# Optimization experiments

Measured on AMD Instinct MI355X. Metric: run time of the kernel, lower is better.

The kernel has to match this reference:

```python
import jax, jax.numpy as jnp
import numpy as np

B, T, C = 2, 2048, 2048
N_HEAD, N_KV_HEAD = 16, 4
HEAD_DIM = C // N_HEAD  # 128
HALF = HEAD_DIM // 2    # 64


def _rms_norm(x):
    # F.rms_norm with no weight: x / sqrt(mean(x^2) + eps), eps = dtype eps
    eps = jnp.finfo(x.dtype).eps
    return x * jax.lax.rsqrt(jnp.mean(x * x, axis=-1, keepdims=True) + eps)


def _rope_apply(x, cos, sin):
    # x: [B, H, T, Hs]; cos/sin: [1, 1, T, Hs/2]
    x1, x2 = x[..., :HALF], x[..., HALF:]
    return jnp.concatenate([x1 * cos - x2 * sin, x1 * sin + x2 * cos], axis=-1)


def setup_inputs() -> dict:
    key = jax.random.key(0)
    ks = jax.random.split(key, 8)
    x = jax.random.normal(ks[0], (B, T, C), dtype=jnp.float32)
    # real RoPE tables (base 10000), shape [1,1,T,HALF]
    inv_freq = 1.0 / (10000.0 ** (np.arange(0, HALF, dtype=np.float32) / HALF))
    t = np.arange(T, dtype=np.float32)
    ang = np.einsum('t,f->tf', t, inv_freq)
    cos = jnp.asarray(np.cos(ang))[None, None]
    sin = jnp.asarray(np.sin(ang))[None, None]
    s = 0.02
    Wq = jax.random.normal(ks[1], (C, N_HEAD * HEAD_DIM), dtype=jnp.float32) * s
    Wk = jax.random.normal(ks[2], (C, N_KV_HEAD * HEAD_DIM), dtype=jnp.float32) * s
    Wv = jax.random.normal(ks[3], (C, N_KV_HEAD * HEAD_DIM), dtype=jnp.float32) * s
    Wo = jax.random.normal(ks[4], (C, C), dtype=jnp.float32) * s
    bo = jnp.zeros((C,), dtype=jnp.float32)
    return {"x": x, "cos": cos, "sin": sin, "Wq": Wq, "Wk": Wk, "Wv": Wv, "Wo": Wo, "bo": bo}


def reference(x, cos, sin, Wq, Wk, Wv, Wo, bo):
    Bq, Tq, Cq = x.shape
    G = N_HEAD // N_KV_HEAD
    # QKV projections (GQA, no bias)
    q = (x @ Wq).reshape(Bq, Tq, N_HEAD, HEAD_DIM)
    k = (x @ Wk).reshape(Bq, Tq, N_KV_HEAD, HEAD_DIM)
    v = (x @ Wv).reshape(Bq, Tq, N_KV_HEAD, HEAD_DIM)
    # QK RMSNorm (over head_dim), then to [B, H, T, Hs]
    q = jnp.transpose(_rms_norm(q), (0, 2, 1, 3))
    k = jnp.transpose(_rms_norm(k), (0, 2, 1, 3))
    v = jnp.transpose(v, (0, 2, 1, 3))
    # RoPE
    q = _rope_apply(q, cos[:, :, :Tq, :], sin[:, :, :Tq, :])
    k = _rope_apply(k, cos[:, :, :Tq, :], sin[:, :, :Tq, :])
    # GQA: repeat kv heads across groups
    k = jnp.repeat(k, G, axis=1)  # [B, H, T, Hs]
    v = jnp.repeat(v, G, axis=1)
    # Causal SDPA
    scale = 1.0 / jnp.sqrt(jnp.asarray(HEAD_DIM, dtype=x.dtype))
    scores = jnp.einsum('bhqd,bhkd->bhqk', q, k) * scale
    causal = jnp.tril(jnp.ones((Tq, Tq), dtype=bool))
    scores = jnp.where(causal, scores, jnp.asarray(-jnp.inf, dtype=scores.dtype))
    attn = jax.nn.softmax(scores, axis=-1)
    y = jnp.einsum('bhqk,bhkd->bhqd', attn, v)
    y = jnp.transpose(y, (0, 2, 1, 3)).reshape(Bq, Tq, Cq)
    return y @ Wo + bo
```

## Files before the change

### kernel.cpp

```cpp
#include <hip/hip_runtime.h>
#include <hip/hip_bf16.h>
#include <math.h>

#define BB 2
#define TT 2048
#define CC 2048
#define NH 16
#define NKV 4
#define HD 128
#define HALF 64
#define MTOT (BB*TT)
#define NQKV (CC + 2*NKV*HD)

typedef unsigned short u16;
typedef __attribute__((ext_vector_type(8))) short bf16x8;
typedef __attribute__((ext_vector_type(4))) float f32x4;

__device__ __forceinline__ u16 f2bf(float f) {
  unsigned u = __float_as_uint(f);
  unsigned r = (u + 0x7FFFu + ((u >> 16) & 1u)) >> 16;
  return (u16)r;
}
__device__ __forceinline__ float bf2f(u16 v) {
  return __uint_as_float(((unsigned)v) << 16);
}

__device__ __forceinline__ void gl_lds16(const void* g, void* l) {
  __builtin_amdgcn_global_load_lds(
      (const __attribute__((address_space(1))) unsigned int*)g,
      (__attribute__((address_space(3))) unsigned int*)l, 16, 0, 0);
}

__global__ __launch_bounds__(256) void prep(
    const float* __restrict__ x, const float* __restrict__ Wq,
    const float* __restrict__ Wk, const float* __restrict__ Wv,
    const float* __restrict__ Wo, u16* __restrict__ xb,
    u16* __restrict__ Wt, u16* __restrict__ Wot) {
  const int z = blockIdx.z;
  const int tx = threadIdx.x, ty = threadIdx.y;
  if (z == 4) {
    const int tid = ty * 32 + tx;
    const int i = (blockIdx.y * 64 + blockIdx.x) * 256 + tid;
    const float4* s4 = (const float4*)x;
    float4 a = s4[(size_t)i * 2], b = s4[(size_t)i * 2 + 1];
    bf16x8 o;
    o[0] = (short)f2bf(a.x); o[1] = (short)f2bf(a.y);
    o[2] = (short)f2bf(a.z); o[3] = (short)f2bf(a.w);
    o[4] = (short)f2bf(b.x); o[5] = (short)f2bf(b.y);
    o[6] = (short)f2bf(b.z); o[7] = (short)f2bf(b.w);
    ((bf16x8*)xb)[i] = o;
    return;
  }
  const float* W; u16* dst; int N; int row_off;
  if (z == 0)      { W = Wq; dst = Wt;  N = 2048; row_off = 0; }
  else if (z == 1) { W = Wk; dst = Wt;  N = 512;  row_off = 2048; }
  else if (z == 2) { W = Wv; dst = Wt;  N = 512;  row_off = 2560; }
  else             { W = Wo; dst = Wot; N = 2048; row_off = 0; }
  const int n0 = blockIdx.x * 32, k0 = blockIdx.y * 32;
  if (n0 >= N) return;
  __shared__ float tile[32][33];
#pragma unroll
  for (int i = 0; i < 4; ++i)
    tile[ty + 8 * i][tx] = W[(size_t)(k0 + ty + 8 * i) * N + n0 + tx];
  __syncthreads();
#pragma unroll
  for (int i = 0; i < 4; ++i)
    dst[(size_t)(row_off + n0 + ty + 8 * i) * CC + k0 + tx] =
        f2bf(tile[tx][ty + 8 * i]);
}

__global__ __launch_bounds__(512, 2) void gemm_8ph(
    const u16* __restrict__ A, const u16* __restrict__ Bt,
    const float* __restrict__ bias, float* __restrict__ C,
    int M, int N, int K, int out_bf16) {
  __shared__ u16 As[32768];
  __shared__ u16 Bs[32768];
  const int tid = threadIdx.x;
  const int w = tid >> 6, lane = tid & 63;
  const int quad = lane >> 4, lo = lane & 15;
  const int wm = w >> 2, wn = w & 3;
  const int bm = blockIdx.y * 256, bn = blockIdx.x * 256;
  const int NT = K >> 6;

  const u16* agp[2][2]; const u16* bgp[2][2];
#pragma unroll
  for (int h = 0; h < 2; ++h)
#pragma unroll
    for (int j = 0; j < 2; ++j) {
      const unsigned X = (unsigned)h * 16384u +
                         (unsigned)((w * 2 + j) * 64 + lane) * 16u;
      const int row = (int)(X >> 7);
      const int ce = (int)(((X & 127u) ^ (((X >> 7) & 7u) << 4)) >> 1);
      agp[h][j] = A  + (size_t)(bm + row) * K + ce;
      bgp[h][j] = Bt + (size_t)(bn + row) * K + ce;
    }
  char* const lAs = (char*)As;
  char* const lBs = (char*)Bs;
  const int woff = w * 2048;

#define STGA(hh, bufp, kt) do { \
    gl_lds16(agp[hh][0] + (size_t)(kt) * 64, lAs + (bufp) * 32768 + (hh) * 16384 + woff); \
    gl_lds16(agp[hh][1] + (size_t)(kt) * 64, lAs + (bufp) * 32768 + (hh) * 16384 + woff + 1024); \
  } while (0)
#define STGB(hh, bufp, kt) do { \
    gl_lds16(bgp[hh][0] + (size_t)(kt) * 64, lBs + (bufp) * 32768 + (hh) * 16384 + woff); \
    gl_lds16(bgp[hh][1] + (size_t)(kt) * 64, lBs + (bufp) * 32768 + (hh) * 16384 + woff + 1024); \
  } while (0)

  const int sw  = (lo & 7) << 4;
  const int co0 = (quad * 16) ^ sw;
  const int co1 = (64 + quad * 16) ^ sw;
  const int aRB = (wm * 128 + lo) * 128;
  const int bRB = (wn * 64 + lo) * 128;

  f32x4 acc[8][4];
#pragma unroll
  for (int ri = 0; ri < 8; ++ri)
#pragma unroll
    for (int ci = 0; ci < 4; ++ci)
#pragma unroll
      for (int r = 0; r < 4; ++r) acc[ri][ci][r] = 0.f;

  STGA(0, 0, 0); STGA(1, 0, 0); STGB(0, 0, 0); STGB(1, 0, 0);
  STGB(0, 1, 1); STGB(1, 1, 1); STGA(0, 1, 1);
  asm volatile("s_waitcnt vmcnt(6)" ::: "memory");
  __builtin_amdgcn_s_barrier();

  for (int t = 0; t < NT; ++t) {
    const int pa = t & 1;
    const char* Ab = lAs + pa * 32768 + aRB;
    const char* Bb = lBs + pa * 32768 + bRB;
    bf16x8 a[4][2], b0[2][2], b1[2][2];

#pragma unroll
    for (int i = 0; i < 4; ++i) {
      a[i][0] = *(const bf16x8*)(Ab + i * 2048 + co0);
      a[i][1] = *(const bf16x8*)(Ab + i * 2048 + co1);
    }
#pragma unroll
    for (int j = 0; j < 2; ++j) {
      b0[j][0] = *(const bf16x8*)(Bb + j * 2048 + co0);
      b0[j][1] = *(const bf16x8*)(Bb + j * 2048 + co1);
    }
    if (t + 1 < NT) STGA(1, (t + 1) & 1, t + 1);
    __builtin_amdgcn_s_barrier();
    asm volatile("s_waitcnt lgkmcnt(0)");
    __builtin_amdgcn_s_setprio(1);
#pragma unroll
    for (int i = 0; i < 4; ++i)
#pragma unroll
      for (int j = 0; j < 2; ++j) {
        acc[i][j] = __builtin_amdgcn_mfma_f32_16x16x32_bf16(a[i][0], b0[j][0], acc[i][j], 0, 0, 0);
        acc[i][j] = __builtin_amdgcn_mfma_f32_16x16x32_bf16(a[i][1], b0[j][1], acc[i][j], 0, 0, 0);
      }
    __builtin_amdgcn_s_setprio(0);
    __builtin_amdgcn_s_barrier();

#pragma unroll
    for (int j = 0; j < 2; ++j) {
      b1[j][0] = *(const bf16x8*)(Bb + 4096 + j * 2048 + co0);
      b1[j][1] = *(const bf16x8*)(Bb + 4096 + j * 2048 + co1);
    }
    __builtin_amdgcn_s_barrier();
    asm volatile("s_waitcnt lgkmcnt(0)");
    __builtin_amdgcn_s_setprio(1);
#pragma unroll
    for (int i = 0; i < 4; ++i)
#pragma unroll
      for (int j = 0; j < 2; ++j) {
        acc[i][2 + j] = __builtin_amdgcn_mfma_f32_16x16x32_bf16(a[i][0], b1[j][0], acc[i][2 + j], 0, 0, 0);
        acc[i][2 + j] = __builtin_amdgcn_mfma_f32_16x16x32_bf16(a[i][1], b1[j][1], acc[i][2 + j], 0, 0, 0);
      }
    __builtin_amdgcn_s_setprio(0);
    __builtin_amdgcn_s_barrier();

#pragma unroll
    for (int i = 0; i < 4; ++i) {
      a[i][0] = *(const bf16x8*)(Ab + 8192 + i * 2048 + co0);
      a[i][1] = *(const bf16x8*)(Ab + 8192 + i * 2048 + co1);
    }
    if (t + 2 < NT) STGB(0, pa, t + 2);
    __builtin_amdgcn_s_barrier();
    asm volatile("s_waitcnt lgkmcnt(0)");
    __builtin_amdgcn_s_setprio(1);
#pragma unroll
    for (int i = 0; i < 4; ++i)
#pragma unroll
      for (int j = 0; j < 2; ++j) {
        acc[4 + i][2 + j] = __builtin_amdgcn_mfma_f32_16x16x32_bf16(a[i][0], b1[j][0], acc[4 + i][2 + j], 0, 0, 0);
        acc[4 + i][2 + j] = __builtin_amdgcn_mfma_f32_16x16x32_bf16(a[i][1], b1[j][1], acc[4 + i][2 + j], 0, 0, 0);
      }
    __builtin_amdgcn_s_setprio(0);
    __builtin_amdgcn_s_barrier();

    if (t + 2 < NT) { STGB(1, pa, t + 2); STGA(0, pa, t + 2); }
    if (t + 2 < NT)      asm volatile("s_waitcnt vmcnt(6)" ::: "memory");
    else if (t + 1 < NT) asm volatile("s_waitcnt vmcnt(0)" ::: "memory");
    __builtin_amdgcn_s_barrier();
    asm volatile("s_waitcnt lgkmcnt(0)");
    __builtin_amdgcn_s_setprio(1);
#pragma unroll
    for (int i = 0; i < 4; ++i)
#pragma unroll
      for (int j = 0; j < 2; ++j) {
        acc[4 + i][j] = __builtin_amdgcn_mfma_f32_16x16x32_bf16(a[i][0], b0[j][0], acc[4 + i][j], 0, 0, 0);
        acc[4 + i][j] = __builtin_amdgcn_mfma_f32_16x16x32_bf16(a[i][1], b0[j][1], acc[4 + i][j], 0, 0, 0);
      }
    __builtin_amdgcn_s_setprio(0);
    __builtin_amdgcn_s_barrier();
  }
#undef STGA
#undef STGB

  const int rbase = bm + wm * 128;
  const int cbase = bn + wn * 64;
#pragma unroll
  for (int ri = 0; ri < 8; ++ri)
#pragma unroll
    for (int ci = 0; ci < 4; ++ci) {
      const int col = cbase + ci * 16 + lo;
      const float bv = bias ? bias[col] : 0.f;
#pragma unroll
      for (int r = 0; r < 4; ++r) {
        const int row = rbase + ri * 16 + quad * 4 + r;
        const float v = acc[ri][ci][r] + bv;
        if (out_bf16) ((u16*)C)[(size_t)row * N + col] = f2bf(v);
        else          C[(size_t)row * N + col] = v;
      }
    }
}

__global__ __launch_bounds__(512, 2) void gemm_n128(
    const u16* __restrict__ A, const u16* __restrict__ Bt,
    const float* __restrict__ bias, float* __restrict__ C,
    int M, int N, int K, int out_bf16) {
  __shared__ u16 As[32768];
  __shared__ u16 Bs[16384];
  const int tid = threadIdx.x;
  const int w = tid >> 6, lane = tid & 63;
  const int quad = lane >> 4, lo = lane & 15;
  const int wm = w >> 1, wn = w & 1;
  const int bm = blockIdx.y * 256, bn = blockIdx.x * 128;
  const int NT = K >> 6;

  const u16* agp[2][2];
#pragma unroll
  for (int h = 0; h < 2; ++h)
#pragma unroll
    for (int j = 0; j < 2; ++j) {
      const unsigned X = (unsigned)h * 16384u +
                         (unsigned)((w * 2 + j) * 64 + lane) * 16u;
      const int row = (int)(X >> 7);
      const int ce = (int)(((X & 127u) ^ (((X >> 7) & 7u) << 4)) >> 1);
      agp[h][j] = A + (size_t)(bm + row) * K + ce;
    }
  const u16* bgp[2];
#pragma unroll
  for (int j = 0; j < 2; ++j) {
    const unsigned X = (unsigned)((w * 2 + j) * 64 + lane) * 16u;
    const int row = (int)(X >> 7);
    const int ce = (int)(((X & 127u) ^ (((X >> 7) & 7u) << 4)) >> 1);
    bgp[j] = Bt + (size_t)(bn + row) * K + ce;
  }
  char* const lAs = (char*)As;
  char* const lBs = (char*)Bs;
  const int woff = w * 2048;

#define STGA_(hh, bufp, kt) do { \
    gl_lds16(agp[hh][0] + (size_t)(kt) * 64, lAs + (bufp) * 32768 + (hh) * 16384 + woff); \
    gl_lds16(agp[hh][1] + (size_t)(kt) * 64, lAs + (bufp) * 32768 + (hh) * 16384 + woff + 1024); \
  } while (0)
#define STGB_(bufp, kt) do { \
    gl_lds16(bgp[0] + (size_t)(kt) * 64, lBs + (bufp) * 16384 + woff); \
    gl_lds16(bgp[1] + (size_t)(kt) * 64, lBs + (bufp) * 16384 + woff + 1024); \
  } while (0)

  const int sw  = (lo & 7) << 4;
  const int co0 = (quad * 16) ^ sw;
  const int co1 = (64 + quad * 16) ^ sw;
  const int aRB = (wm * 64 + lo) * 128;
  const int bRB = (wn * 64 + lo) * 128;

  f32x4 acc[4][4];
#pragma unroll
  for (int i = 0; i < 4; ++i)
#pragma unroll
    for (int ci = 0; ci < 4; ++ci)
#pragma unroll
      for (int r = 0; r < 4; ++r) acc[i][ci][r] = 0.f;

  STGA_(0, 0, 0); STGA_(1, 0, 0); STGB_(0, 0);
  STGB_(1, 1); STGA_(0, 1, 1);
  asm volatile("s_waitcnt vmcnt(4)" ::: "memory");
  __builtin_amdgcn_s_barrier();

  for (int t = 0; t < NT; ++t) {
    const int pa = t & 1;
    const char* Ab = lAs + pa * 32768 + aRB;
    const char* Bb = lBs + pa * 16384 + bRB;
    bf16x8 a[4][2], b[4][2];
#pragma unroll
    for (int i = 0; i < 4; ++i) {
      a[i][0] = *(const bf16x8*)(Ab + i * 2048 + co0);
      a[i][1] = *(const bf16x8*)(Ab + i * 2048 + co1);
    }
#pragma unroll
    for (int ci = 0; ci < 4; ++ci) {
      b[ci][0] = *(const bf16x8*)(Bb + ci * 2048 + co0);
      b[ci][1] = *(const bf16x8*)(Bb + ci * 2048 + co1);
    }
    if (t + 1 < NT) STGA_(1, (t + 1) & 1, t + 1);
    asm volatile("s_waitcnt lgkmcnt(0)");
    __builtin_amdgcn_s_barrier();
    __builtin_amdgcn_s_setprio(1);
#pragma unroll
    for (int i = 0; i < 4; ++i)
#pragma unroll
      for (int ci = 0; ci < 2; ++ci) {
        acc[i][ci] = __builtin_amdgcn_mfma_f32_16x16x32_bf16(a[i][0], b[ci][0], acc[i][ci], 0, 0, 0);
        acc[i][ci] = __builtin_amdgcn_mfma_f32_16x16x32_bf16(a[i][1], b[ci][1], acc[i][ci], 0, 0, 0);
      }
    __builtin_amdgcn_s_setprio(0);
    if (t + 2 < NT) { STGB_(pa, t + 2); STGA_(0, pa, t + 2); }
    if (t + 2 < NT)      asm volatile("s_waitcnt vmcnt(4)" ::: "memory");
    else if (t + 1 < NT) asm volatile("s_waitcnt vmcnt(0)" ::: "memory");
    __builtin_amdgcn_s_setprio(1);
#pragma unroll
    for (int i = 0; i < 4; ++i)
#pragma unroll
      for (int ci = 2; ci < 4; ++ci) {
        acc[i][ci] = __builtin_amdgcn_mfma_f32_16x16x32_bf16(a[i][0], b[ci][0], acc[i][ci], 0, 0, 0);
        acc[i][ci] = __builtin_amdgcn_mfma_f32_16x16x32_bf16(a[i][1], b[ci][1], acc[i][ci], 0, 0, 0);
      }
    __builtin_amdgcn_s_setprio(0);
    __builtin_amdgcn_s_barrier();
  }
#undef STGA_
#undef STGB_

  const int rbase = bm + wm * 64;
  const int cbase = bn + wn * 64;
#pragma unroll
  for (int i = 0; i < 4; ++i)
#pragma unroll
    for (int ci = 0; ci < 4; ++ci) {
      const int col = cbase + ci * 16 + lo;
      const float bv = bias ? bias[col] : 0.f;
#pragma unroll
      for (int r = 0; r < 4; ++r) {
        const int row = rbase + i * 16 + quad * 4 + r;
        const float v = acc[i][ci][r] + bv;
        if (out_bf16) ((u16*)C)[(size_t)row * N + col] = f2bf(v);
        else          C[(size_t)row * N + col] = v;
      }
    }
}

__global__ __launch_bounds__(256) void qkv_post(
    const u16* __restrict__ qkv_lin, const float* __restrict__ cosp,
    const float* __restrict__ sinp, u16* __restrict__ q, u16* __restrict__ k) {
  const int bt = blockIdx.x;
  const int hh = blockIdx.y * 4 + (threadIdx.x >> 6);
  const int lane = threadIdx.x & 63;
  const int t = bt & (TT - 1), b = bt >> 11;
  const int col = (hh < NH) ? hh * HD : CC + (hh - NH) * HD;
  const u16* src = qkv_lin + (size_t)bt * NQKV + col;
  float v1 = bf2f(src[lane]), v2 = bf2f(src[lane + 64]);
  float ss = v1 * v1 + v2 * v2;
#pragma unroll
  for (int mm = 1; mm < 64; mm <<= 1) ss += __shfl_xor(ss, mm, 64);
  float rms = rsqrtf(ss * (1.f / 128.f) + 1.1920929e-7f);
  float c = cosp[t * HALF + lane], s = sinp[t * HALF + lane];
  float o1 = v1 * rms * c - v2 * rms * s;
  float o2 = v1 * rms * s + v2 * rms * c;
  if (hh < NH) {
    u16* dst = q + (((size_t)(b * NH + hh)) * TT + t) * HD;
    dst[lane] = f2bf(o1); dst[lane + 64] = f2bf(o2);
  } else {
    u16* dst = k + (((size_t)(b * NKV + (hh - NH))) * TT + t) * HD;
    dst[lane] = f2bf(o1); dst[lane + 64] = f2bf(o2);
  }
}

__global__ __launch_bounds__(256) void v_transpose(
    const u16* __restrict__ qkv_lin, u16* __restrict__ vt) {
  __shared__ u16 tile[32][33];
  const int t0 = blockIdx.x * 32, d0 = blockIdx.y * 32;
  const int p = blockIdx.z;
  const int b = p >> 2, kv = p & 3;
  const int tx = threadIdx.x, ty = threadIdx.y;
#pragma unroll
  for (int i = 0; i < 4; ++i)
    tile[ty + 8 * i][tx] =
        qkv_lin[(size_t)(b * TT + t0 + ty + 8 * i) * NQKV + CC + NKV * HD + kv * HD + d0 + tx];
  __syncthreads();
  const int tperm = ((tx >> 2) & 3) * 8 + (tx & 3) + 4 * ((tx >> 4) & 1);
#pragma unroll
  for (int i = 0; i < 4; ++i)
    vt[((size_t)p * HD + d0 + ty + 8 * i) * TT + t0 + tperm] = tile[tx][ty + 8 * i];
}

__device__ __forceinline__ void softmax_pack(
    const f32x4* sacc, float& l_lane, bf16x8* ap, int rowq, int t0,
    bool diag, int quad) {
  const float cc = 0.12751744050808612f;
  float e[4][4];
  if (diag) {
#pragma unroll
    for (int ct = 0; ct < 4; ++ct)
#pragma unroll
      for (int r = 0; r < 4; ++r) {
        float v = __builtin_amdgcn_exp2f(sacc[ct][r] * cc);
        if (t0 + ct * 16 + quad * 4 + r > rowq) v = 0.f;
        l_lane += v; e[ct][r] = v;
      }
  } else {
#pragma unroll
    for (int ct = 0; ct < 4; ++ct)
#pragma unroll
      for (int r = 0; r < 4; ++r) {
        float v = __builtin_amdgcn_exp2f(sacc[ct][r] * cc);
        l_lane += v; e[ct][r] = v;
      }
  }
#pragma unroll
  for (int k2 = 0; k2 < 2; ++k2) {
    bf16x8 ch;
#pragma unroll
    for (int j = 0; j < 8; ++j)
      ch[j] = (short)f2bf(e[k2 * 2 + (j >> 2)][j & 3]);
    ap[k2] = ch;
  }
}

__global__ __launch_bounds__(256, 2) void attn_mfma(
    const u16* __restrict__ Qb, const u16* __restrict__ Kb,
    const u16* __restrict__ Vt, u16* __restrict__ Y) {
  __shared__ u16 Ks[2][8192];
  __shared__ u16 Vs[2][8192];

  const int qt = blockIdx.x;
  const int bh = blockIdx.y;
  const int b = bh >> 4, h = bh & 15, kvh = h >> 2;
  const int tid = threadIdx.x;
  const int wave = tid >> 6, lane = tid & 63;
  const int quad = lane >> 4, lo = lane & 15;

  const int rowsA = qt * 64, rowsB = (31 - qt) * 64;
  const u16* Qg = Qb + (size_t)(b * NH + h) * TT * HD;
  const u16* Kg = Kb + (size_t)(b * NKV + kvh) * TT * HD;
  const u16* Vg = Vt + (size_t)(b * NKV + kvh) * HD * TT;

  bf16x8 aq[2][4];
#pragma unroll
  for (int kc = 0; kc < 4; ++kc) {
    aq[0][kc] = *(const bf16x8*)(Qg + (size_t)(rowsA + wave * 16 + lo) * HD + kc * 32 + quad * 8);
    aq[1][kc] = *(const bf16x8*)(Qg + (size_t)(rowsB + wave * 16 + lo) * HD + kc * 32 + quad * 8);
  }

  const u16* kgp[4]; const u16* vgp[4];
  u16* klp[2][4]; u16* vlp[2][4];
#pragma unroll
  for (int c = 0; c < 4; ++c) {
    const int s = wave * 4 + c;
    const int ct = s >> 2, kq = s & 3;
    kgp[c] = Kg + (size_t)(ct * 16 + lo) * HD + kq * 32 + quad * 8;
    const int dt = s >> 1, k2 = s & 1;
    vgp[c] = Vg + (size_t)(dt * 16 + lo) * TT + k2 * 32 + quad * 8;
    klp[0][c] = &Ks[0][s * 512]; klp[1][c] = &Ks[1][s * 512];
    vlp[0][c] = &Vs[0][s * 512]; vlp[1][c] = &Vs[1][s * 512];
  }

  f32x4 oacc[2][8];
#pragma unroll
  for (int rb = 0; rb < 2; ++rb)
#pragma unroll
    for (int dt = 0; dt < 8; ++dt)
#pragma unroll
      for (int r = 0; r < 4; ++r) oacc[rb][dt][r] = 0.f;
  float l_lane[2] = {0.f, 0.f};

  const int ntiles = 32 - qt;
  const int rowqA = rowsA + wave * 16 + lo;
  const int rowqB = rowsB + wave * 16 + lo;

#pragma unroll
  for (int c = 0; c < 4; ++c) {
    gl_lds16(kgp[c], klp[0][c]); kgp[c] += 64 * HD;
    gl_lds16(vgp[c], vlp[0][c]); vgp[c] += 64;
  }

  for (int nt = 0; nt < ntiles; ++nt) {
    const int par = nt & 1;
    __syncthreads();
    if (nt + 1 < ntiles) {
#pragma unroll
      for (int c = 0; c < 4; ++c) {
        gl_lds16(kgp[c], klp[par ^ 1][c]); kgp[c] += 64 * HD;
        gl_lds16(vgp[c], vlp[par ^ 1][c]); vgp[c] += 64;
      }
    }
    const u16* ksb = Ks[par];
    const u16* vsb = Vs[par];
    const int t0 = nt * 64;
    const bool act0 = (nt <= qt);

    f32x4 sacc[2][4];
#pragma unroll
    for (int rb = 0; rb < 2; ++rb)
#pragma unroll
      for (int ct = 0; ct < 4; ++ct)
#pragma unroll
        for (int r = 0; r < 4; ++r) sacc[rb][ct][r] = 0.f;
#pragma unroll
    for (int ct = 0; ct < 4; ++ct)
#pragma unroll
      for (int kc = 0; kc < 4; ++kc) {
        bf16x8 bk = *(const bf16x8*)&ksb[(ct * 4 + kc) * 512 + lane * 8];
        sacc[1][ct] = __builtin_amdgcn_mfma_f32_16x16x32_bf16(bk, aq[1][kc], sacc[1][ct], 0, 0, 0);
        if (act0)
          sacc[0][ct] = __builtin_amdgcn_mfma_f32_16x16x32_bf16(bk, aq[0][kc], sacc[0][ct], 0, 0, 0);
      }

    bf16x8 ap[2][2];
    softmax_pack(sacc[1], l_lane[1], ap[1], rowqB, t0,
                 t0 + 63 > rowsB + wave * 16, quad);
    if (act0)
      softmax_pack(sacc[0], l_lane[0], ap[0], rowqA, t0,
                   t0 + 63 > rowsA + wave * 16, quad);

#pragma unroll
    for (int dt = 0; dt < 8; ++dt)
#pragma unroll
      for (int k2 = 0; k2 < 2; ++k2) {
        bf16x8 bv = *(const bf16x8*)&vsb[(dt * 2 + k2) * 512 + lane * 8];
        oacc[1][dt] = __builtin_amdgcn_mfma_f32_16x16x32_bf16(ap[1][k2], bv, oacc[1][dt], 0, 0, 0);
        if (act0)
          oacc[0][dt] = __builtin_amdgcn_mfma_f32_16x16x32_bf16(ap[0][k2], bv, oacc[0][dt], 0, 0, 0);
      }
  }

  float linv[2][4];
#pragma unroll
  for (int rb = 0; rb < 2; ++rb) {
    float l = l_lane[rb];
    l += __shfl_xor(l, 16, 64);
    l += __shfl_xor(l, 32, 64);
    l = 1.f / l;
#pragma unroll
    for (int r = 0; r < 4; ++r)
      linv[rb][r] = __shfl(l, quad * 4 + r, 64);
  }
#pragma unroll
  for (int rb = 0; rb < 2; ++rb) {
    const int rows = (rb == 0) ? rowsA : rowsB;
    const size_t row0 = (size_t)b * TT + rows + wave * 16 + quad * 4;
#pragma unroll
    for (int dt = 0; dt < 8; ++dt)
#pragma unroll
      for (int r = 0; r < 4; ++r)
        Y[(row0 + r) * CC + h * HD + dt * 16 + lo] = f2bf(oacc[rb][dt][r] * linv[rb][r]);
  }
}

extern "C" void kernel_launch(void* const* d_in, const int* in_sizes, int n_in,
                              void* d_out, int out_size, void* d_ws, size_t ws_size,
                              hipStream_t stream) {
  (void)in_sizes; (void)n_in; (void)out_size; (void)ws_size;
  const float* x    = (const float*)d_in[0];
  const float* cosp = (const float*)d_in[1];
  const float* sinp = (const float*)d_in[2];
  const float* Wq   = (const float*)d_in[3];
  const float* Wk   = (const float*)d_in[4];
  const float* Wv   = (const float*)d_in[5];
  const float* Wo   = (const float*)d_in[6];
  const float* bo   = (const float*)d_in[7];
  float* out = (float*)d_out;
  char* ws = (char*)d_ws;

  const size_t MB = 1024 * 1024;
  u16* xb      = (u16*)(ws);
  u16* Wt      = (u16*)(ws + 16 * MB);
  u16* qkv_lin = (u16*)(ws + 28 * MB);
  u16* Wot     = (u16*)(ws + 52 * MB);
  u16* qb_buf  = (u16*)(ws);
  u16* kb      = (u16*)(ws + 16 * MB);
  u16* vt      = (u16*)(ws + 20 * MB);
  u16* y       = (u16*)(ws + 28 * MB);

  prep<<<dim3(64, 64, 5), dim3(32, 8), 0, stream>>>(x, Wq, Wk, Wv, Wo, xb, Wt, Wot);

  gemm_8ph<<<dim3(NQKV / 256, MTOT / 256), 512, 0, stream>>>(
      xb, Wt, nullptr, (float*)qkv_lin, MTOT, NQKV, CC, 1);

  qkv_post<<<dim3(MTOT, 5), 256, 0, stream>>>(qkv_lin, cosp, sinp, qb_buf, kb);

  v_transpose<<<dim3(TT / 32, HD / 32, BB * NKV), dim3(32, 8), 0, stream>>>(qkv_lin, vt);

  attn_mfma<<<dim3(16, BB * NH), 256, 0, stream>>>(qb_buf, kb, vt, y);

  gemm_n128<<<dim3(CC / 128, MTOT / 256), 512, 0, stream>>>(
      y, Wot, bo, out, MTOT, CC, CC, 0);
}
```

Before: 310.3 us.

## Split attention block into two wave groups, one per paired query tile

The attention kernel now launches 512 threads per block instead of 256. Each half of the block (4 waves) handles one of the two paired causal query tiles, where before every wave processed both tiles. This cuts per-wave register state (single oacc/sacc set), which should allow higher occupancy, and lets the two tiles run in parallel on separate waves. K/V staging is split across 8 waves, and s_setprio is added around the MFMA sections to favour matrix issue. The risk is that the wave group for the short tile sits idle on later iterations while still paying for the block-wide syncthreads.

Result: no change. 307.0 us (-1.1%).

```diff
diff --git a/kernel.cpp b/kernel.cpp
--- a/kernel.cpp
+++ b/kernel.cpp
@@ -433,7 +433,7 @@
   }
 }
 
-__global__ __launch_bounds__(256, 2) void attn_mfma(
+__global__ __launch_bounds__(512, 4) void attn_mfma(
     const u16* __restrict__ Qb, const u16* __restrict__ Kb,
     const u16* __restrict__ Vt, u16* __restrict__ Y) {
   __shared__ u16 Ks[2][8192];
@@ -444,25 +444,24 @@
   const int b = bh >> 4, h = bh & 15, kvh = h >> 2;
   const int tid = threadIdx.x;
   const int wave = tid >> 6, lane = tid & 63;
+  const int wg = wave >> 2, wv = wave & 3;
   const int quad = lane >> 4, lo = lane & 15;
 
-  const int rowsA = qt * 64, rowsB = (31 - qt) * 64;
+  const int rows = (wg == 0) ? qt * 64 : (31 - qt) * 64;
   const u16* Qg = Qb + (size_t)(b * NH + h) * TT * HD;
   const u16* Kg = Kb + (size_t)(b * NKV + kvh) * TT * HD;
   const u16* Vg = Vt + (size_t)(b * NKV + kvh) * HD * TT;
 
-  bf16x8 aq[2][4];
-#pragma unroll
-  for (int kc = 0; kc < 4; ++kc) {
-    aq[0][kc] = *(const bf16x8*)(Qg + (size_t)(rowsA + wave * 16 + lo) * HD + kc * 32 + quad * 8);
-    aq[1][kc] = *(const bf16x8*)(Qg + (size_t)(rowsB + wave * 16 + lo) * HD + kc * 32 + quad * 8);
-  }
-
-  const u16* kgp[4]; const u16* vgp[4];
-  u16* klp[2][4]; u16* vlp[2][4];
-#pragma unroll
-  for (int c = 0; c < 4; ++c) {
-    const int s = wave * 4 + c;
+  bf16x8 aq[4];
+#pragma unroll
+  for (int kc = 0; kc < 4; ++kc)
+    aq[kc] = *(const bf16x8*)(Qg + (size_t)(rows + wv * 16 + lo) * HD + kc * 32 + quad * 8);
+
+  const u16* kgp[2]; const u16* vgp[2];
+  u16* klp[2][2]; u16* vlp[2][2];
+#pragma unroll
+  for (int c = 0; c < 2; ++c) {
+    const int s = wave * 2 + c;
     const int ct = s >> 2, kq = s & 3;
     kgp[c] = Kg + (size_t)(ct * 16 + lo) * HD + kq * 32 + quad * 8;
     const int dt = s >> 1, k2 = s & 1;
@@ -471,21 +470,18 @@
     vlp[0][c] = &Vs[0][s * 512]; vlp[1][c] = &Vs[1][s * 512];
   }
 
-  f32x4 oacc[2][8];
-#pragma unroll
-  for (int rb = 0; rb < 2; ++rb)
-#pragma unroll
-    for (int dt = 0; dt < 8; ++dt)
-#pragma unroll
-      for (int r = 0; r < 4; ++r) oacc[rb][dt][r] = 0.f;
-  float l_lane[2] = {0.f, 0.f};
+  f32x4 oacc[8];
+#pragma unroll
+  for (int dt = 0; dt < 8; ++dt)
+#pragma unroll
+    for (int r = 0; r < 4; ++r) oacc[dt][r] = 0.f;
+  float l_lane = 0.f;
 
   const int ntiles = 32 - qt;
-  const int rowqA = rowsA + wave * 16 + lo;
-  const int rowqB = rowsB + wave * 16 + lo;
-
-#pragma unroll
-  for (int c = 0; c < 4; ++c) {
+  const int rowq = rows + wv * 16 + lo;
+
+#pragma unroll
+  for (int c = 0; c < 2; ++c) {
     gl_lds16(kgp[c], klp[0][c]); kgp[c] += 64 * HD;
     gl_lds16(vgp[c], vlp[0][c]); vgp[c] += 64;
   }
@@ -495,72 +491,61 @@
     __syncthreads();
     if (nt + 1 < ntiles) {
 #pragma unroll
-      for (int c = 0; c < 4; ++c) {
+      for (int c = 0; c < 2; ++c) {
         gl_lds16(kgp[c], klp[par ^ 1][c]); kgp[c] += 64 * HD;
         gl_lds16(vgp[c], vlp[par ^ 1][c]); vgp[c] += 64;
       }
     }
-    const u16* ksb = Ks[par];
-    const u16* vsb = Vs[par];
-    const int t0 = nt * 64;
-    const bool act0 = (nt <= qt);
-
-    f32x4 sacc[2][4];
-#pragma unroll
-    for (int rb = 0; rb < 2; ++rb)
+    const bool act = (wg == 1) || (nt <= qt);
+    if (act) {
+      const u16* ksb = Ks[par];
+      const u16* vsb = Vs[par];
+      const int t0 = nt * 64;
+
+      f32x4 sacc[4];
 #pragma unroll
       for (int ct = 0; ct < 4; ++ct)
 #pragma unroll
-        for (int r = 0; r < 4; ++r) sacc[rb][ct][r] = 0.f;
-#pragma unroll
-    for (int ct = 0; ct < 4; ++ct)
-#pragma unroll
-      for (int kc = 0; kc < 4; ++kc) {
-        bf16x8 bk = *(const bf16x8*)&ksb[(ct * 4 + kc) * 512 + lane * 8];
-        sacc[1][ct] = __builtin_amdgcn_mfma_f32_16x16x32_bf16(bk, aq[1][kc], sacc[1][ct], 0, 0, 0);
-        if (act0)
-          sacc[0][ct] = __builtin_amdgcn_mfma_f32_16x16x32_bf16(bk, aq[0][kc], sacc[0][ct], 0, 0, 0);
-      }
-
-    bf16x8 ap[2][2];
-    softmax_pack(sacc[1], l_lane[1], ap[1], rowqB, t0,
-                 t0 + 63 > rowsB + wave * 16, quad);
-    if (act0)
-      softmax_pack(sacc[0], l_lane[0], ap[0], rowqA, t0,
-                   t0 + 63 > rowsA + wave * 16, quad);
-
-#pragma unroll
-    for (int dt = 0; dt < 8; ++dt)
-#pragma unroll
-      for (int k2 = 0; k2 < 2; ++k2) {
-        bf16x8 bv = *(const bf16x8*)&vsb[(dt * 2 + k2) * 512 + lane * 8];
-        oacc[1][dt] = __builtin_amdgcn_mfma_f32_16x16x32_bf16(ap[1][k2], bv, oacc[1][dt], 0, 0, 0);
-        if (act0)
-          oacc[0][dt] = __builtin_amdgcn_mfma_f32_16x16x32_bf16(ap[0][k2], bv, oacc[0][dt], 0, 0, 0);
-      }
-  }
-
-  float linv[2][4];
-#pragma unroll
-  for (int rb = 0; rb < 2; ++rb) {
-    float l = l_lane[rb];
-    l += __shfl_xor(l, 16, 64);
-    l += __shfl_xor(l, 32, 64);
-    l = 1.f / l;
+        for (int r = 0; r < 4; ++r) sacc[ct][r] = 0.f;
+      __builtin_amdgcn_s_setprio(1);
+#pragma unroll
+      for (int ct = 0; ct < 4; ++ct)
+#pragma unroll
+        for (int kc = 0; kc < 4; ++kc) {
+          bf16x8 bk = *(const bf16x8*)&ksb[(ct * 4 + kc) * 512 + lane * 8];
+          sacc[ct] = __builtin_amdgcn_mfma_f32_16x16x32_bf16(bk, aq[kc], sacc[ct], 0, 0, 0);
+        }
+      __builtin_amdgcn_s_setprio(0);
+
+      bf16x8 ap[2];
+      softmax_pack(sacc, l_lane, ap, rowq, t0, t0 + 63 > rows + wv * 16, quad);
+
+      __builtin_amdgcn_s_setprio(1);
+#pragma unroll
+      for (int dt = 0; dt < 8; ++dt)
+#pragma unroll
+        for (int k2 = 0; k2 < 2; ++k2) {
+          bf16x8 bv = *(const bf16x8*)&vsb[(dt * 2 + k2) * 512 + lane * 8];
+          oacc[dt] = __builtin_amdgcn_mfma_f32_16x16x32_bf16(ap[k2], bv, oacc[dt], 0, 0, 0);
+        }
+      __builtin_amdgcn_s_setprio(0);
+    }
+  }
+
+  float l = l_lane;
+  l += __shfl_xor(l, 16, 64);
+  l += __shfl_xor(l, 32, 64);
+  l = 1.f / l;
+  float linv[4];
+#pragma unroll
+  for (int r = 0; r < 4; ++r)
+    linv[r] = __shfl(l, quad * 4 + r, 64);
+  const size_t row0 = (size_t)b * TT + rows + wv * 16 + quad * 4;
+#pragma unroll
+  for (int dt = 0; dt < 8; ++dt)
 #pragma unroll
     for (int r = 0; r < 4; ++r)
-      linv[rb][r] = __shfl(l, quad * 4 + r, 64);
-  }
-#pragma unroll
-  for (int rb = 0; rb < 2; ++rb) {
-    const int rows = (rb == 0) ? rowsA : rowsB;
-    const size_t row0 = (size_t)b * TT + rows + wave * 16 + quad * 4;
-#pragma unroll
-    for (int dt = 0; dt < 8; ++dt)
-#pragma unroll
-      for (int r = 0; r < 4; ++r)
-        Y[(row0 + r) * CC + h * HD + dt * 16 + lo] = f2bf(oacc[rb][dt][r] * linv[rb][r]);
-  }
+      Y[(row0 + r) * CC + h * HD + dt * 16 + lo] = f2bf(oacc[dt][r] * linv[r]);
 }
 
 extern "C" void kernel_launch(void* const* d_in, const int* in_sizes, int n_in,
@@ -597,7 +582,7 @@
 
   v_transpose<<<dim3(TT / 32, HD / 32, BB * NKV), dim3(32, 8), 0, stream>>>(qkv_lin, vt);
 
-  attn_mfma<<<dim3(16, BB * NH), 256, 0, stream>>>(qb_buf, kb, vt, y);
+  attn_mfma<<<dim3(16, BB * NH), 512, 0, stream>>>(qb_buf, kb, vt, y);
 
   gemm_n128<<<dim3(CC / 128, MTOT / 256), 512, 0, stream>>>(
       y, Wot, bo, out, MTOT, CC, CC, 0);
```
